# Optimization experiments

Measured on AMD Instinct MI355X. Metric: run time of the kernel, lower is better.

The kernel has to match this reference:

```python
import jax, jax.numpy as jnp
import numpy as np


def _ap_class_loss(s_plus, s_minus):
    """AP rank loss for one class.

    s_plus:  [P] positive scores sorted DESCENDING (grads flow through sort gather)
    s_minus: [N] negative scores sorted ASCENDING  (grads flow through sort gather)

    The original torch code computes the optimal interleaving rank of each
    negative with a recursive quickselect divide-and-conquer. Because the
    optimal rank is monotone in the negative's score (the property the
    divide-and-conquer exploits), each negative's rank can equivalently be
    computed independently: for the negative of ascending rank j (1-indexed),
    delta_k = 1/(P*(j+k)) - 2*(s_plus[k-1] - s_minus[j-1])/(P*N),  k=1..P,
    opt_j = argmax over r in [1, P+1] of sum_{k>=r} delta_k (first max on ties),
    which is exactly opt_j() evaluated on the full range.
    """
    P = s_plus.shape[0]
    N = s_minus.shape[0]
    Pf, Nf = float(P), float(N)
    j = jnp.arange(1, N + 1, dtype=jnp.float32)[:, None]   # [N,1] ascending rank
    k = jnp.arange(1, P + 1, dtype=jnp.float32)[None, :]   # [1,P]
    # delta[m, k-1] for negative m (ascending) vs positive k (descending)
    delta = (1.0 / (j + k)) / Pf - 2.0 * (s_plus[None, :] - s_minus[:, None]) / (Pf * Nf)
    dz = jnp.concatenate([delta, jnp.zeros((N, 1), delta.dtype)], axis=1)  # [N,P+1]
    # suffix[m, u] = sum_{i>=u} dz[m, i]  (matches flip-cumsum-flip in torch)
    suffix = jnp.cumsum(dz[:, ::-1], axis=1)[:, ::-1]
    opt = 1 + jnp.argmax(suffix, axis=1)                    # [N] int in [1, P+1]
    opt_f = jax.lax.stop_gradient(opt.astype(jnp.float32))
    # r_plus[i] = 1 + |{m : opt_m <= i+1}| via cumulative histogram of opt values
    hist = jnp.zeros(P + 2, jnp.float32).at[opt].add(1.0)
    cum = jnp.cumsum(hist)
    r_plus = 1.0 + cum[1:P + 1]                             # [P], thresholds 1..P
    i_arr = jnp.arange(P, dtype=jnp.float32)
    Delta_R_R_star = 1.0 - jnp.sum((i_arr + 1.0) / (i_arr + r_plus)) / Pf
    c_plus = Nf + 2.0 - 2.0 * r_plus                        # detached in torch
    c_minus = Pf + 2.0 - 2.0 * opt_f
    F_R = jnp.dot(s_plus, c_plus) + jnp.dot(s_minus, c_minus)
    # c_plus_star = N*ones, c_minus_star = -P*ones
    F_R_star = Nf * jnp.sum(s_plus) - Pf * jnp.sum(s_minus)
    return jax.lax.stop_gradient(Delta_R_R_star) + (F_R - F_R_star) / (Pf * Nf)


def _ap_loss(scores, pos_neg):
    total = jnp.zeros((), scores.dtype)
    for c, (pos, neg) in enumerate(pos_neg):
        if pos.size == 0 or neg.size == 0:
            continue  # torch returns 0 * s_plus.sum()
        col = scores[:, c]
        sp = col[pos]
        sm = col[neg]
        sp = sp[jnp.argsort(-sp)]   # descending; detached sort idx, grad via gather
        sm = sm[jnp.argsort(sm)]    # ascending (quickselect partial sort, same pairing)
        total = total + _ap_class_loss(sp, sm)
    return total / len(pos_neg)


def setup_inputs() -> dict:
    key = jax.random.key(0)
    k1, k2 = jax.random.split(key)
    C, n_classes = 16384, 16
    scores = jax.random.normal(k1, (C, n_classes), dtype=jnp.float32)
    class_labels = jax.random.randint(k2, (C,), 0, n_classes, dtype=jnp.int32)
    return {"scores": scores, "class_labels": class_labels}


def reference(scores, class_labels):
    labels = np.asarray(class_labels)
    n_classes = scores.shape[1]
    pos_neg = [(np.nonzero(labels == c)[0], np.nonzero(labels != c)[0])
               for c in range(n_classes)]
    return _ap_loss(scores, pos_neg)
```

## Files before the change

### kernel.cpp

```cpp
#include <hip/hip_runtime.h>
#include <stdint.h>

#define C_ITEMS 16384
#define NCLS 16
#define HSTRIDE 16386

static const size_t OFF_COL  = 0;
static const size_t OFF_SPOS = 1u << 20;
static const size_t OFF_SNEG = 2u << 20;
static const size_t OFF_PACK = 3u << 20;
static const size_t OFF_HIST = 4u << 20;
static const size_t OFF_CNT  = OFF_HIST + (size_t)NCLS * HSTRIDE * 4;
static const size_t OFF_ACCS = OFF_CNT + 64;
static const size_t OFF_ACCV = OFF_ACCS + 128;
static const size_t OFF_TOT  = OFF_ACCV + 128;
static const size_t OFF_PC   = OFF_TOT + 8;
static const size_t OFF_H1   = (OFF_PC + 64 + 255) & ~(size_t)255;
static const size_t OFF_PPK  = OFF_H1 + (((size_t)NCLS << 16) * 4);
static const size_t ZERO_BYTES = OFF_PPK - OFF_HIST;

__device__ __forceinline__ unsigned ordkey(float f) {
  unsigned b = __float_as_uint(f);
  return (b & 0x80000000u) ? ~b : (b | 0x80000000u);
}

__global__ void k_zero(unsigned* p, int n) {
  int stride = gridDim.x * blockDim.x;
  for (int t = blockIdx.x * blockDim.x + threadIdx.x; t < n; t += stride) p[t] = 0u;
}

__global__ void k_prep(const float* __restrict__ scores, const int* __restrict__ labels,
                       float* __restrict__ col, unsigned* __restrict__ h1) {
  int t = blockIdx.x * 256 + threadIdx.x;
  float v = scores[t];
  int i = t >> 4, c = t & 15;
  col[(c << 14) | i] = v;
  if (labels[i] != c)
    atomicAdd(&h1[(c << 16) + (ordkey(v) >> 16)], 1u);
}

__global__ void k_poscollect(const float* __restrict__ scores, const int* __restrict__ labels,
                             unsigned* __restrict__ pcnt, unsigned long long* __restrict__ ppk) {
  __shared__ unsigned lc[NCLS];
  __shared__ unsigned base[NCLS];
  int tid = threadIdx.x;
  if (tid < NCLS) lc[tid] = 0;
  __syncthreads();
  int i = blockIdx.x * 256 + tid;
  int c = labels[i] & 15;
  float v = scores[i * NCLS + c];
  unsigned loc = atomicAdd(&lc[c], 1u);
  __syncthreads();
  if (tid < NCLS) base[tid] = lc[tid] ? atomicAdd(&pcnt[tid], lc[tid]) : 0u;
  __syncthreads();
  ppk[(c << 14) + base[c] + loc] = ((unsigned long long)(~ordkey(v)) << 32) | (unsigned)i;
}

#define PCAP 4096
__global__ void k_posrank2(const float* __restrict__ scores,
                           const unsigned long long* __restrict__ ppk,
                           const unsigned* __restrict__ pcnt, float* __restrict__ spos) {
  int c = blockIdx.y;
  unsigned P = pcnt[c];
  int tid = threadIdx.x;
  __shared__ unsigned long long pk[PCAP];
  const unsigned long long* src = ppk + ((size_t)c << 14);
  if (P <= PCAP) {
    for (unsigned t = tid; t < P; t += 256) pk[t] = src[t];
    __syncthreads();
    for (unsigned q = blockIdx.x * 256 + tid; q < P; q += gridDim.x * 256) {
      unsigned long long k64 = pk[q];
      unsigned cq = 0;
      for (unsigned t = 0; t < P; ++t) cq += (pk[t] < k64) ? 1u : 0u;
      unsigned i = (unsigned)(k64 & 0xFFFFFFFFu);
      spos[(c << 14) + cq] = scores[i * NCLS + c];
    }
  } else {
    for (unsigned q = blockIdx.x * 256 + tid; q < P; q += gridDim.x * 256) {
      unsigned long long k64 = src[q];
      unsigned cq = 0;
      for (unsigned t = 0; t < P; ++t) cq += (src[t] < k64) ? 1u : 0u;
      unsigned i = (unsigned)(k64 & 0xFFFFFFFFu);
      spos[(c << 14) + cq] = scores[i * NCLS + c];
    }
  }
}

__global__ void k_scan1(unsigned* __restrict__ h1) {
  int c = blockIdx.x;
  unsigned* h = h1 + ((size_t)c << 16);
  int tid = threadIdx.x;
  unsigned base = (unsigned)tid << 6;
  unsigned s = 0;
  for (int q = 0; q < 64; ++q) s += h[base + q];
  __shared__ unsigned part[1024];
  part[tid] = s;
  __syncthreads();
  for (int off = 1; off < 1024; off <<= 1) {
    unsigned v = (tid >= off) ? part[tid - off] : 0u;
    __syncthreads();
    part[tid] += v;
    __syncthreads();
  }
  unsigned running = part[tid] - s;
  for (int q = 0; q < 64; ++q) {
    unsigned tmp = h[base + q];
    h[base + q] = running;
    running += tmp;
  }
}

__global__ void k_scatter(const float* __restrict__ col, const int* __restrict__ labels,
                          unsigned* __restrict__ h1, unsigned* __restrict__ pack) {
  int t = blockIdx.x * 256 + threadIdx.x;
  int c = t >> 14, i = t & 16383;
  if (labels[i] != c) {
    unsigned k = ordkey(col[t]);
    unsigned p = atomicAdd(&h1[(c << 16) + (k >> 16)], 1u);
    pack[(c << 14) + p] = (k << 16) | (unsigned)i;
  }
}

__global__ void k_rankfine(const float* __restrict__ col, const int* __restrict__ labels,
                           const unsigned* __restrict__ h1, const unsigned* __restrict__ pack,
                           float* __restrict__ sneg) {
  int t = blockIdx.x * 256 + threadIdx.x;
  int c = t >> 14, i = t & 16383;
  if (labels[i] != c) {
    float v = col[t];
    unsigned k = ordkey(v);
    unsigned b = k >> 16;
    const unsigned* hb = h1 + ((size_t)c << 16);
    unsigned start = b ? hb[b - 1] : 0u;
    unsigned end = hb[b];
    unsigned mine = (k << 16) | (unsigned)i;
    const unsigned* pk = pack + (c << 14);
    unsigned cnt = start;
    for (unsigned q = start; q < end; ++q) cnt += (pk[q] < mine) ? 1u : 0u;
    sneg[(c << 14) + cnt] = v;
  }
}

#define SCAP 2048
#define HCAP 2048
#define ABITS 6
#define ASTEP 64

__global__ void k_anchor(const unsigned* __restrict__ counts, const float* __restrict__ spos,
                         const float* __restrict__ sneg, unsigned* __restrict__ aopt) {
  int c = blockIdx.y;
  int P = (int)counts[c];
  int N = C_ITEMS - P;
  if (P == 0 || N == 0) return;
  int tid = threadIdx.x;
  __shared__ float sp[SCAP];
  int stageN = (P <= SCAP) ? P : 0;
  for (int t = tid; t < stageN; t += 256) sp[t] = spos[(c << 14) + t];
  __syncthreads();
  int T = (N + ASTEP - 1) / ASTEP + 1;
  float invP = 1.0f / (float)P;
  float coef = 2.0f / ((float)P * (float)N);
  for (int t = tid; t < T; t += 256) {
    int j0 = min(t * ASTEP, N - 1);
    float v = sneg[(c << 14) + j0];
    float a = coef * v;
    float fcnt = (float)(j0 + P + 1);
    float s = 0.0f, best = 0.0f;
    int besti = P;
    if (P <= SCAP) {
      for (int q = P - 1; q >= 0; --q) {
        float spv = sp[q];
        float r = __builtin_amdgcn_rcpf(fcnt);
        float delta = fmaf(invP, r, fmaf(-coef, spv, a));
        s += delta;
        if (s >= best) { best = s; besti = q; }
        fcnt -= 1.0f;
      }
    } else {
      const float* spg = spos + ((size_t)c << 14);
      for (int q = P - 1; q >= 0; --q) {
        float spv = spg[q];
        float r = __builtin_amdgcn_rcpf(fcnt);
        float delta = fmaf(invP, r, fmaf(-coef, spv, a));
        s += delta;
        if (s >= best) { best = s; besti = q; }
        fcnt -= 1.0f;
      }
    }
    aopt[(c << 9) + t] = (unsigned)(besti + 1);
  }
}

__global__ void k_optB(const unsigned* __restrict__ counts, const float* __restrict__ spos,
                       const float* __restrict__ sneg, const unsigned* __restrict__ aopt,
                       unsigned* __restrict__ hist, double* __restrict__ accS,
                       double* __restrict__ accV) {
  int c = blockIdx.y;
  int P = (int)counts[c];
  int N = C_ITEMS - P;
  if (P == 0 || N == 0) return;
  int tid = threadIdx.x;
  int j0 = blockIdx.x * 256 + tid;
  bool active = (j0 < N);
  __shared__ float sp[SCAP];
  __shared__ unsigned lh[HCAP];
  __shared__ double red[256];
  int stageN = (P <= SCAP) ? P : 0;
  for (int t = tid; t < stageN; t += 256) sp[t] = spos[(c << 14) + t];
  for (int t = tid; t < HCAP; t += 256) lh[t] = 0u;
  __syncthreads();
  int opt = P + 1;
  float v = 0.0f;
  if (active) {
    v = sneg[(c << 14) + j0];
    int g = j0 >> ABITS;
    int hiA = (int)aopt[(c << 9) + g];
    if ((j0 & (ASTEP - 1)) == 0) {
      opt = hiA;
    } else {
      int loA = (int)aopt[(c << 9) + g + 1];
      int hi = min(hiA + 2, P + 1);
      int lo = max(loA - 2, 1);
      float invP = 1.0f / (float)P;
      float coef = 2.0f / ((float)P * (float)N);
      float a = coef * v;
      float s = 0.0f, best = 0.0f;
      int bestr = hi;
      float fcnt = (float)(j0 + hi);
      if (P <= SCAP) {
        for (int k = hi - 1; k >= lo; --k) {
          float spv = sp[k - 1];
          float r = __builtin_amdgcn_rcpf(fcnt);
          float delta = fmaf(invP, r, fmaf(-coef, spv, a));
          s += delta;
          if (s >= best) { best = s; bestr = k; }
          fcnt -= 1.0f;
        }
      } else {
        const float* spg = spos + ((size_t)c << 14);
        for (int k = hi - 1; k >= lo; --k) {
          float spv = spg[k - 1];
          float r = __builtin_amdgcn_rcpf(fcnt);
          float delta = fmaf(invP, r, fmaf(-coef, spv, a));
          s += delta;
          if (s >= best) { best = s; bestr = k; }
          fcnt -= 1.0f;
        }
      }
      opt = bestr;
    }
  }
  if (P + 2 <= HCAP) {
    if (active) atomicAdd(&lh[opt], 1u);
    __syncthreads();
    for (int t = tid; t < P + 2; t += 256)
      if (lh[t]) atomicAdd(&hist[c * HSTRIDE + t], lh[t]);
  } else {
    if (active) atomicAdd(&hist[c * HSTRIDE + opt], 1u);
  }
  double cm = active ? (double)(P + 2 - 2 * opt) * (double)v : 0.0;
  double sv = active ? (double)v : 0.0;
  red[tid] = cm; __syncthreads();
  for (int sh = 128; sh > 0; sh >>= 1) { if (tid < sh) red[tid] += red[tid + sh]; __syncthreads(); }
  if (tid == 0) atomicAdd(&accS[c], red[0]);
  __syncthreads();
  red[tid] = sv; __syncthreads();
  for (int sh = 128; sh > 0; sh >>= 1) { if (tid < sh) red[tid] += red[tid + sh]; __syncthreads(); }
  if (tid == 0) atomicAdd(&accV[c], red[0]);
}

__global__ void k_finalize(const unsigned* __restrict__ counts, const unsigned* __restrict__ hist,
                           const float* __restrict__ spos, const double* __restrict__ accS,
                           const double* __restrict__ accV, double* __restrict__ total) {
  int c = blockIdx.x;
  int tid = threadIdx.x;
  int P = (int)counts[c];
  int N = C_ITEMS - P;
  if (P == 0 || N == 0) return;
  __shared__ unsigned sc[256];
  __shared__ double red[256];
  const unsigned* h = hist + c * HSTRIDE;
  int M = P + 1;
  int L = (M + 255) / 256;
  int o0 = 1 + tid * L;
  int o1 = min(o0 + L, P + 2);
  unsigned part = 0;
  for (int o = o0; o < o1; ++o) part += h[o];
  sc[tid] = part;
  __syncthreads();
  if (tid == 0) {
    unsigned runp = 0;
    for (int t = 0; t < 256; ++t) { unsigned tmp = sc[t]; sc[t] = runp; runp += tmp; }
  }
  __syncthreads();
  unsigned run = sc[tid];
  double a1 = 0.0, a2 = 0.0, a3 = 0.0;
  for (int o = o0; o < o1; ++o) {
    run += h[o];
    if (o <= P) {
      int k0 = o - 1;
      double rp = 1.0 + (double)run;
      double spv = (double)spos[(c << 14) + k0];
      a1 += (double)(k0 + 1) / ((double)k0 + rp);
      a2 += spv * ((double)N + 2.0 - 2.0 * rp);
      a3 += spv;
    }
  }
  red[tid] = a1; __syncthreads();
  for (int s = 128; s > 0; s >>= 1) { if (tid < s) red[tid] += red[tid + s]; __syncthreads(); }
  double r1 = red[0]; __syncthreads();
  red[tid] = a2; __syncthreads();
  for (int s = 128; s > 0; s >>= 1) { if (tid < s) red[tid] += red[tid + s]; __syncthreads(); }
  double r2 = red[0]; __syncthreads();
  red[tid] = a3; __syncthreads();
  for (int s = 128; s > 0; s >>= 1) { if (tid < s) red[tid] += red[tid + s]; __syncthreads(); }
  double r3 = red[0];
  if (tid == 0) {
    double Pd = (double)P, Nd = (double)N;
    double FR  = r2 + accS[c];
    double FRs = Nd * r3 - Pd * accV[c];
    double lc  = (1.0 - r1 / Pd) + (FR - FRs) / (Pd * Nd);
    atomicAdd(total, lc);
  }
}

__global__ void k_out(const double* __restrict__ total, float* __restrict__ out) {
  out[0] = (float)(total[0] / (double)NCLS);
}

extern "C" void kernel_launch(void* const* d_in, const int* in_sizes, int n_in,
                              void* d_out, int out_size, void* d_ws, size_t ws_size,
                              hipStream_t stream) {
  (void)in_sizes; (void)n_in; (void)out_size; (void)ws_size;
  const float* scores = (const float*)d_in[0];
  const int* labels = (const int*)d_in[1];
  float* out = (float*)d_out;
  char* ws = (char*)d_ws;
  float* col      = (float*)(ws + OFF_COL);
  float* spos     = (float*)(ws + OFF_SPOS);
  float* sneg     = (float*)(ws + OFF_SNEG);
  unsigned* pack  = (unsigned*)(ws + OFF_PACK);
  unsigned* hist  = (unsigned*)(ws + OFF_HIST);
  double* accS    = (double*)(ws + OFF_ACCS);
  double* accV    = (double*)(ws + OFF_ACCV);
  double* total   = (double*)(ws + OFF_TOT);
  unsigned* pcnt  = (unsigned*)(ws + OFF_PC);
  unsigned* h1    = (unsigned*)(ws + OFF_H1);
  unsigned long long* ppk = (unsigned long long*)(ws + OFF_PPK);
  unsigned* aopt  = (unsigned*)(ws + OFF_PPK);

  int zn = (int)(ZERO_BYTES / 4);
  k_zero<<<1024, 256, 0, stream>>>(hist, zn);
  k_prep<<<1024, 256, 0, stream>>>(scores, labels, col, h1);
  k_poscollect<<<64, 256, 0, stream>>>(scores, labels, pcnt, ppk);
  k_posrank2<<<dim3(16, NCLS), 256, 0, stream>>>(scores, ppk, pcnt, spos);
  k_scan1<<<NCLS, 1024, 0, stream>>>(h1);
  k_scatter<<<1024, 256, 0, stream>>>(col, labels, h1, pack);
  k_rankfine<<<1024, 256, 0, stream>>>(col, labels, h1, pack, sneg);
  k_anchor<<<dim3(1, NCLS), 256, 0, stream>>>(pcnt, spos, sneg, aopt);
  k_optB<<<dim3(64, NCLS), 256, 0, stream>>>(pcnt, spos, sneg, aopt, hist, accS, accV);
  k_finalize<<<NCLS, 256, 0, stream>>>(pcnt, hist, spos, accS, accV, total);
  k_out<<<1, 1, 0, stream>>>(total, out);
}
```

Baseline: 215.9 us.

## Fuse per-class sort, positive ranking and anchor search into one LDS-resident kernel

Merges the column transpose with positive collection, and collapses positive ranking, the negative radix histogram, scan, scatter, fine ranking and anchor search into one 1024-thread block per class that keeps its histogram and pack buffers in LDS. The final reduction and output write are folded together using a last-block counter. This is meant to remove launch overhead and global atomics/round-trips between stages. The cost is that only 16 blocks run the sort phase, which limits parallelism on a large GPU, and a large dynamic LDS allocation is required.

```diff
diff --git a/kernel.cpp b/kernel.cpp
--- a/kernel.cpp
+++ b/kernel.cpp
@@ -4,20 +4,22 @@
 #define C_ITEMS 16384
 #define NCLS 16
 #define HSTRIDE 16386
+#define NB 16384
+#define BSH 18
 
 static const size_t OFF_COL  = 0;
 static const size_t OFF_SPOS = 1u << 20;
 static const size_t OFF_SNEG = 2u << 20;
-static const size_t OFF_PACK = 3u << 20;
+static const size_t OFF_AOPT = 3u << 20;
 static const size_t OFF_HIST = 4u << 20;
 static const size_t OFF_CNT  = OFF_HIST + (size_t)NCLS * HSTRIDE * 4;
 static const size_t OFF_ACCS = OFF_CNT + 64;
 static const size_t OFF_ACCV = OFF_ACCS + 128;
 static const size_t OFF_TOT  = OFF_ACCV + 128;
 static const size_t OFF_PC   = OFF_TOT + 8;
-static const size_t OFF_H1   = (OFF_PC + 64 + 255) & ~(size_t)255;
-static const size_t OFF_PPK  = OFF_H1 + (((size_t)NCLS << 16) * 4);
-static const size_t ZERO_BYTES = OFF_PPK - OFF_HIST;
+static const size_t ZERO_END = OFF_PC + 64;
+static const size_t ZERO_BYTES = ZERO_END - OFF_HIST;
+static const size_t OFF_PPK  = 6u << 20;
 
 __device__ __forceinline__ unsigned ordkey(float f) {
   unsigned b = __float_as_uint(f);
@@ -29,168 +31,170 @@
   for (int t = blockIdx.x * blockDim.x + threadIdx.x; t < n; t += stride) p[t] = 0u;
 }
 
-__global__ void k_prep(const float* __restrict__ scores, const int* __restrict__ labels,
-                       float* __restrict__ col, unsigned* __restrict__ h1) {
-  int t = blockIdx.x * 256 + threadIdx.x;
-  float v = scores[t];
-  int i = t >> 4, c = t & 15;
-  col[(c << 14) | i] = v;
-  if (labels[i] != c)
-    atomicAdd(&h1[(c << 16) + (ordkey(v) >> 16)], 1u);
-}
-
-__global__ void k_poscollect(const float* __restrict__ scores, const int* __restrict__ labels,
-                             unsigned* __restrict__ pcnt, unsigned long long* __restrict__ ppk) {
+__global__ void k_prep2(const float* __restrict__ scores, const int* __restrict__ labels,
+                        float* __restrict__ col, unsigned* __restrict__ pcnt,
+                        unsigned long long* __restrict__ ppk) {
   __shared__ unsigned lc[NCLS];
   __shared__ unsigned base[NCLS];
   int tid = threadIdx.x;
   if (tid < NCLS) lc[tid] = 0;
   __syncthreads();
   int i = blockIdx.x * 256 + tid;
+  const float4* rp = (const float4*)(scores + (size_t)i * NCLS);
+  float4 r0 = rp[0], r1 = rp[1], r2 = rp[2], r3 = rp[3];
   int c = labels[i] & 15;
-  float v = scores[i * NCLS + c];
   unsigned loc = atomicAdd(&lc[c], 1u);
   __syncthreads();
   if (tid < NCLS) base[tid] = lc[tid] ? atomicAdd(&pcnt[tid], lc[tid]) : 0u;
   __syncthreads();
+  float v = scores[(size_t)i * NCLS + c];
   ppk[(c << 14) + base[c] + loc] = ((unsigned long long)(~ordkey(v)) << 32) | (unsigned)i;
-}
-
-#define PCAP 4096
-__global__ void k_posrank2(const float* __restrict__ scores,
-                           const unsigned long long* __restrict__ ppk,
-                           const unsigned* __restrict__ pcnt, float* __restrict__ spos) {
-  int c = blockIdx.y;
-  unsigned P = pcnt[c];
+  col[(0 << 14) + i] = r0.x;  col[(1 << 14) + i] = r0.y;
+  col[(2 << 14) + i] = r0.z;  col[(3 << 14) + i] = r0.w;
+  col[(4 << 14) + i] = r1.x;  col[(5 << 14) + i] = r1.y;
+  col[(6 << 14) + i] = r1.z;  col[(7 << 14) + i] = r1.w;
+  col[(8 << 14) + i] = r2.x;  col[(9 << 14) + i] = r2.y;
+  col[(10 << 14) + i] = r2.z; col[(11 << 14) + i] = r2.w;
+  col[(12 << 14) + i] = r3.x; col[(13 << 14) + i] = r3.y;
+  col[(14 << 14) + i] = r3.z; col[(15 << 14) + i] = r3.w;
+}
+
+#define SCAP 2048
+#define ASTEP 64
+#define ABITS 6
+
+extern __shared__ char smem_ms[];
+
+__global__ __launch_bounds__(1024) void k_megasort(
+    const float* __restrict__ col, const int* __restrict__ labels,
+    const unsigned* __restrict__ pcnt, const unsigned long long* __restrict__ ppk,
+    float* __restrict__ spos, float* __restrict__ sneg, unsigned* __restrict__ aopt) {
+  int c = blockIdx.x;
   int tid = threadIdx.x;
-  __shared__ unsigned long long pk[PCAP];
-  const unsigned long long* src = ppk + ((size_t)c << 14);
-  if (P <= PCAP) {
-    for (unsigned t = tid; t < P; t += 256) pk[t] = src[t];
-    __syncthreads();
-    for (unsigned q = blockIdx.x * 256 + tid; q < P; q += gridDim.x * 256) {
+  int P = (int)pcnt[c];
+  int N = C_ITEMS - P;
+  unsigned* hist = (unsigned*)smem_ms;
+  unsigned* pack = (unsigned*)(smem_ms + (size_t)NB * 4);
+  float*    sp   = (float*)(smem_ms + (size_t)NB * 4 + 65536);
+  unsigned long long* pk = (unsigned long long*)pack;
+  __shared__ unsigned part[1024];
+
+  bool small = (P > 0 && P <= SCAP);
+  if (small) {
+    const unsigned long long* src = ppk + ((size_t)c << 14);
+    for (int t = tid; t < P; t += 1024) pk[t] = src[t];
+    __syncthreads();
+    for (int q = tid; q < P; q += 1024) {
       unsigned long long k64 = pk[q];
       unsigned cq = 0;
-      for (unsigned t = 0; t < P; ++t) cq += (pk[t] < k64) ? 1u : 0u;
+      for (int t = 0; t < P; ++t) cq += (pk[t] < k64) ? 1u : 0u;
       unsigned i = (unsigned)(k64 & 0xFFFFFFFFu);
-      spos[(c << 14) + cq] = scores[i * NCLS + c];
-    }
-  } else {
-    for (unsigned q = blockIdx.x * 256 + tid; q < P; q += gridDim.x * 256) {
+      float v = col[(c << 14) + (int)i];
+      sp[cq] = v;
+      spos[(c << 14) + (int)cq] = v;
+    }
+  } else if (P > 0) {
+    const unsigned long long* src = ppk + ((size_t)c << 14);
+    for (int q = tid; q < P; q += 1024) {
       unsigned long long k64 = src[q];
       unsigned cq = 0;
-      for (unsigned t = 0; t < P; ++t) cq += (src[t] < k64) ? 1u : 0u;
+      for (int t = 0; t < P; ++t) cq += (src[t] < k64) ? 1u : 0u;
       unsigned i = (unsigned)(k64 & 0xFFFFFFFFu);
-      spos[(c << 14) + cq] = scores[i * NCLS + c];
-    }
-  }
-}
-
-__global__ void k_scan1(unsigned* __restrict__ h1) {
-  int c = blockIdx.x;
-  unsigned* h = h1 + ((size_t)c << 16);
-  int tid = threadIdx.x;
-  unsigned base = (unsigned)tid << 6;
-  unsigned s = 0;
-  for (int q = 0; q < 64; ++q) s += h[base + q];
-  __shared__ unsigned part[1024];
-  part[tid] = s;
-  __syncthreads();
-  for (int off = 1; off < 1024; off <<= 1) {
-    unsigned v = (tid >= off) ? part[tid - off] : 0u;
-    __syncthreads();
-    part[tid] += v;
-    __syncthreads();
-  }
-  unsigned running = part[tid] - s;
-  for (int q = 0; q < 64; ++q) {
-    unsigned tmp = h[base + q];
-    h[base + q] = running;
-    running += tmp;
-  }
-}
-
-__global__ void k_scatter(const float* __restrict__ col, const int* __restrict__ labels,
-                          unsigned* __restrict__ h1, unsigned* __restrict__ pack) {
-  int t = blockIdx.x * 256 + threadIdx.x;
-  int c = t >> 14, i = t & 16383;
-  if (labels[i] != c) {
-    unsigned k = ordkey(col[t]);
-    unsigned p = atomicAdd(&h1[(c << 16) + (k >> 16)], 1u);
-    pack[(c << 14) + p] = (k << 16) | (unsigned)i;
-  }
-}
-
-__global__ void k_rankfine(const float* __restrict__ col, const int* __restrict__ labels,
-                           const unsigned* __restrict__ h1, const unsigned* __restrict__ pack,
-                           float* __restrict__ sneg) {
-  int t = blockIdx.x * 256 + threadIdx.x;
-  int c = t >> 14, i = t & 16383;
-  if (labels[i] != c) {
-    float v = col[t];
-    unsigned k = ordkey(v);
-    unsigned b = k >> 16;
-    const unsigned* hb = h1 + ((size_t)c << 16);
-    unsigned start = b ? hb[b - 1] : 0u;
-    unsigned end = hb[b];
-    unsigned mine = (k << 16) | (unsigned)i;
-    const unsigned* pk = pack + (c << 14);
-    unsigned cnt = start;
-    for (unsigned q = start; q < end; ++q) cnt += (pk[q] < mine) ? 1u : 0u;
-    sneg[(c << 14) + cnt] = v;
-  }
-}
-
-#define SCAP 2048
+      spos[(c << 14) + (int)cq] = col[(c << 14) + (int)i];
+    }
+  }
+  __syncthreads();
+
+  for (int b = tid; b < NB; b += 1024) hist[b] = 0u;
+  __syncthreads();
+  if (N > 0)
+    for (int i = tid; i < C_ITEMS; i += 1024)
+      if (labels[i] != c) atomicAdd(&hist[ordkey(col[(c << 14) + i]) >> BSH], 1u);
+  __syncthreads();
+
+  {
+    int base = tid * (NB / 1024);
+    unsigned s = 0;
+    for (int q = 0; q < NB / 1024; ++q) s += hist[base + q];
+    part[tid] = s;
+    __syncthreads();
+    for (int off = 1; off < 1024; off <<= 1) {
+      unsigned v = (tid >= off) ? part[tid - off] : 0u;
+      __syncthreads();
+      part[tid] += v;
+      __syncthreads();
+    }
+    unsigned running = part[tid] - s;
+    for (int q = 0; q < NB / 1024; ++q) {
+      unsigned tmp = hist[base + q];
+      hist[base + q] = running;
+      running += tmp;
+    }
+  }
+  __syncthreads();
+
+  if (N > 0)
+    for (int i = tid; i < C_ITEMS; i += 1024)
+      if (labels[i] != c) {
+        unsigned k = ordkey(col[(c << 14) + i]);
+        unsigned p = atomicAdd(&hist[k >> BSH], 1u);
+        pack[p] = (k << 14) | (unsigned)i;
+      }
+  __syncthreads();
+
+  if (N > 0)
+    for (int i = tid; i < C_ITEMS; i += 1024)
+      if (labels[i] != c) {
+        float v = col[(c << 14) + i];
+        unsigned k = ordkey(v);
+        unsigned b = k >> BSH;
+        unsigned start = b ? hist[b - 1] : 0u;
+        unsigned end = hist[b];
+        unsigned mine = (k << 14) | (unsigned)i;
+        unsigned cnt = start;
+        for (unsigned q = start; q < end; ++q) cnt += (pack[q] < mine) ? 1u : 0u;
+        sneg[(c << 14) + (int)cnt] = v;
+      }
+  __threadfence_block();
+  __syncthreads();
+
+  if (P > 0 && N > 0) {
+    int T = (N + ASTEP - 1) / ASTEP + 1;
+    float invP = 1.0f / (float)P;
+    float coef = 2.0f / ((float)P * (float)N);
+    for (int t = tid; t < T; t += 1024) {
+      int j0 = min(t * ASTEP, N - 1);
+      float v = sneg[(c << 14) + j0];
+      float a = coef * v;
+      float fcnt = (float)(j0 + P + 1);
+      float s = 0.0f, best = 0.0f;
+      int besti = P;
+      if (P <= SCAP) {
+        for (int q = P - 1; q >= 0; --q) {
+          float spv = sp[q];
+          float r = __builtin_amdgcn_rcpf(fcnt);
+          float delta = fmaf(invP, r, fmaf(-coef, spv, a));
+          s += delta;
+          if (s >= best) { best = s; besti = q; }
+          fcnt -= 1.0f;
+        }
+      } else {
+        const float* spg = spos + ((size_t)c << 14);
+        for (int q = P - 1; q >= 0; --q) {
+          float spv = spg[q];
+          float r = __builtin_amdgcn_rcpf(fcnt);
+          float delta = fmaf(invP, r, fmaf(-coef, spv, a));
+          s += delta;
+          if (s >= best) { best = s; besti = q; }
+          fcnt -= 1.0f;
+        }
+      }
+      aopt[(c << 9) + t] = (unsigned)(besti + 1);
+    }
+  }
+}
+
 #define HCAP 2048
-#define ABITS 6
-#define ASTEP 64
-
-__global__ void k_anchor(const unsigned* __restrict__ counts, const float* __restrict__ spos,
-                         const float* __restrict__ sneg, unsigned* __restrict__ aopt) {
-  int c = blockIdx.y;
-  int P = (int)counts[c];
-  int N = C_ITEMS - P;
-  if (P == 0 || N == 0) return;
-  int tid = threadIdx.x;
-  __shared__ float sp[SCAP];
-  int stageN = (P <= SCAP) ? P : 0;
-  for (int t = tid; t < stageN; t += 256) sp[t] = spos[(c << 14) + t];
-  __syncthreads();
-  int T = (N + ASTEP - 1) / ASTEP + 1;
-  float invP = 1.0f / (float)P;
-  float coef = 2.0f / ((float)P * (float)N);
-  for (int t = tid; t < T; t += 256) {
-    int j0 = min(t * ASTEP, N - 1);
-    float v = sneg[(c << 14) + j0];
-    float a = coef * v;
-    float fcnt = (float)(j0 + P + 1);
-    float s = 0.0f, best = 0.0f;
-    int besti = P;
-    if (P <= SCAP) {
-      for (int q = P - 1; q >= 0; --q) {
-        float spv = sp[q];
-        float r = __builtin_amdgcn_rcpf(fcnt);
-        float delta = fmaf(invP, r, fmaf(-coef, spv, a));
-        s += delta;
-        if (s >= best) { best = s; besti = q; }
-        fcnt -= 1.0f;
-      }
-    } else {
-      const float* spg = spos + ((size_t)c << 14);
-      for (int q = P - 1; q >= 0; --q) {
-        float spv = spg[q];
-        float r = __builtin_amdgcn_rcpf(fcnt);
-        float delta = fmaf(invP, r, fmaf(-coef, spv, a));
-        s += delta;
-        if (s >= best) { best = s; besti = q; }
-        fcnt -= 1.0f;
-      }
-    }
-    aopt[(c << 9) + t] = (unsigned)(besti + 1);
-  }
-}
-
 __global__ void k_optB(const unsigned* __restrict__ counts, const float* __restrict__ spos,
                        const float* __restrict__ sneg, const unsigned* __restrict__ aopt,
                        unsigned* __restrict__ hist, double* __restrict__ accS,
@@ -269,63 +273,70 @@
   if (tid == 0) atomicAdd(&accV[c], red[0]);
 }
 
-__global__ void k_finalize(const unsigned* __restrict__ counts, const unsigned* __restrict__ hist,
-                           const float* __restrict__ spos, const double* __restrict__ accS,
-                           const double* __restrict__ accV, double* __restrict__ total) {
+__global__ void k_fin(const unsigned* __restrict__ counts, const unsigned* __restrict__ hist,
+                      const float* __restrict__ spos, const double* __restrict__ accS,
+                      const double* __restrict__ accV, double* __restrict__ total,
+                      unsigned* __restrict__ done, float* __restrict__ out) {
   int c = blockIdx.x;
   int tid = threadIdx.x;
   int P = (int)counts[c];
   int N = C_ITEMS - P;
-  if (P == 0 || N == 0) return;
   __shared__ unsigned sc[256];
   __shared__ double red[256];
-  const unsigned* h = hist + c * HSTRIDE;
-  int M = P + 1;
-  int L = (M + 255) / 256;
-  int o0 = 1 + tid * L;
-  int o1 = min(o0 + L, P + 2);
-  unsigned part = 0;
-  for (int o = o0; o < o1; ++o) part += h[o];
-  sc[tid] = part;
-  __syncthreads();
+  double lc = 0.0;
+  if (P > 0 && N > 0) {
+    const unsigned* h = hist + c * HSTRIDE;
+    int M = P + 1;
+    int L = (M + 255) / 256;
+    int o0 = 1 + tid * L;
+    int o1 = min(o0 + L, P + 2);
+    unsigned part = 0;
+    for (int o = o0; o < o1; ++o) part += h[o];
+    sc[tid] = part;
+    __syncthreads();
+    if (tid == 0) {
+      unsigned runp = 0;
+      for (int t = 0; t < 256; ++t) { unsigned tmp = sc[t]; sc[t] = runp; runp += tmp; }
+    }
+    __syncthreads();
+    unsigned run = sc[tid];
+    double a1 = 0.0, a2 = 0.0, a3 = 0.0;
+    for (int o = o0; o < o1; ++o) {
+      run += h[o];
+      if (o <= P) {
+        int k0 = o - 1;
+        double rp = 1.0 + (double)run;
+        double spv = (double)spos[(c << 14) + k0];
+        a1 += (double)(k0 + 1) / ((double)k0 + rp);
+        a2 += spv * ((double)N + 2.0 - 2.0 * rp);
+        a3 += spv;
+      }
+    }
+    red[tid] = a1; __syncthreads();
+    for (int s = 128; s > 0; s >>= 1) { if (tid < s) red[tid] += red[tid + s]; __syncthreads(); }
+    double r1 = red[0]; __syncthreads();
+    red[tid] = a2; __syncthreads();
+    for (int s = 128; s > 0; s >>= 1) { if (tid < s) red[tid] += red[tid + s]; __syncthreads(); }
+    double r2 = red[0]; __syncthreads();
+    red[tid] = a3; __syncthreads();
+    for (int s = 128; s > 0; s >>= 1) { if (tid < s) red[tid] += red[tid + s]; __syncthreads(); }
+    double r3 = red[0];
+    if (tid == 0) {
+      double Pd = (double)P, Nd = (double)N;
+      double FR  = r2 + accS[c];
+      double FRs = Nd * r3 - Pd * accV[c];
+      lc = (1.0 - r1 / Pd) + (FR - FRs) / (Pd * Nd);
+    }
+  }
   if (tid == 0) {
-    unsigned runp = 0;
-    for (int t = 0; t < 256; ++t) { unsigned tmp = sc[t]; sc[t] = runp; runp += tmp; }
-  }
-  __syncthreads();
-  unsigned run = sc[tid];
-  double a1 = 0.0, a2 = 0.0, a3 = 0.0;
-  for (int o = o0; o < o1; ++o) {
-    run += h[o];
-    if (o <= P) {
-      int k0 = o - 1;
-      double rp = 1.0 + (double)run;
-      double spv = (double)spos[(c << 14) + k0];
-      a1 += (double)(k0 + 1) / ((double)k0 + rp);
-      a2 += spv * ((double)N + 2.0 - 2.0 * rp);
-      a3 += spv;
-    }
-  }
-  red[tid] = a1; __syncthreads();
-  for (int s = 128; s > 0; s >>= 1) { if (tid < s) red[tid] += red[tid + s]; __syncthreads(); }
-  double r1 = red[0]; __syncthreads();
-  red[tid] = a2; __syncthreads();
-  for (int s = 128; s > 0; s >>= 1) { if (tid < s) red[tid] += red[tid + s]; __syncthreads(); }
-  double r2 = red[0]; __syncthreads();
-  red[tid] = a3; __syncthreads();
-  for (int s = 128; s > 0; s >>= 1) { if (tid < s) red[tid] += red[tid + s]; __syncthreads(); }
-  double r3 = red[0];
-  if (tid == 0) {
-    double Pd = (double)P, Nd = (double)N;
-    double FR  = r2 + accS[c];
-    double FRs = Nd * r3 - Pd * accV[c];
-    double lc  = (1.0 - r1 / Pd) + (FR - FRs) / (Pd * Nd);
-    atomicAdd(total, lc);
-  }
-}
-
-__global__ void k_out(const double* __restrict__ total, float* __restrict__ out) {
-  out[0] = (float)(total[0] / (double)NCLS);
+    if (P > 0 && N > 0) atomicAdd(total, lc);
+    __threadfence();
+    unsigned d = atomicAdd(done, 1u);
+    if (d == NCLS - 1) {
+      double t = atomicAdd(total, 0.0);
+      out[0] = (float)(t / (double)NCLS);
+    }
+  }
 }
 
 extern "C" void kernel_launch(void* const* d_in, const int* in_sizes, int n_in,
@@ -339,26 +350,27 @@
   float* col      = (float*)(ws + OFF_COL);
   float* spos     = (float*)(ws + OFF_SPOS);
   float* sneg     = (float*)(ws + OFF_SNEG);
-  unsigned* pack  = (unsigned*)(ws + OFF_PACK);
+  unsigned* aopt  = (unsigned*)(ws + OFF_AOPT);
   unsigned* hist  = (unsigned*)(ws + OFF_HIST);
+  unsigned* done  = (unsigned*)(ws + OFF_CNT);
   double* accS    = (double*)(ws + OFF_ACCS);
   double* accV    = (double*)(ws + OFF_ACCV);
   double* total   = (double*)(ws + OFF_TOT);
   unsigned* pcnt  = (unsigned*)(ws + OFF_PC);
-  unsigned* h1    = (unsigned*)(ws + OFF_H1);
   unsigned long long* ppk = (unsigned long long*)(ws + OFF_PPK);
-  unsigned* aopt  = (unsigned*)(ws + OFF_PPK);
+
+  size_t msLds = (size_t)NB * 4 + 65536 + 8192;
+  static bool attr_done = false;
+  if (!attr_done) {
+    (void)hipFuncSetAttribute((const void*)k_megasort,
+                              hipFuncAttributeMaxDynamicSharedMemorySize, (int)msLds);
+    attr_done = true;
+  }
 
   int zn = (int)(ZERO_BYTES / 4);
-  k_zero<<<1024, 256, 0, stream>>>(hist, zn);
-  k_prep<<<1024, 256, 0, stream>>>(scores, labels, col, h1);
-  k_poscollect<<<64, 256, 0, stream>>>(scores, labels, pcnt, ppk);
-  k_posrank2<<<dim3(16, NCLS), 256, 0, stream>>>(scores, ppk, pcnt, spos);
-  k_scan1<<<NCLS, 1024, 0, stream>>>(h1);
-  k_scatter<<<1024, 256, 0, stream>>>(col, labels, h1, pack);
-  k_rankfine<<<1024, 256, 0, stream>>>(col, labels, h1, pack, sneg);
-  k_anchor<<<dim3(1, NCLS), 256, 0, stream>>>(pcnt, spos, sneg, aopt);
+  k_zero<<<256, 256, 0, stream>>>(hist, zn);
+  k_prep2<<<64, 256, 0, stream>>>(scores, labels, col, pcnt, ppk);
+  k_megasort<<<NCLS, 1024, msLds, stream>>>(col, labels, pcnt, ppk, spos, sneg, aopt);
   k_optB<<<dim3(64, NCLS), 256, 0, stream>>>(pcnt, spos, sneg, aopt, hist, accS, accV);
-  k_finalize<<<NCLS, 256, 0, stream>>>(pcnt, hist, spos, accS, accV, total);
-  k_out<<<1, 1, 0, stream>>>(total, out);
-}
+  k_fin<<<NCLS, 256, 0, stream>>>(pcnt, hist, spos, accS, accV, total, done, out);
+}
```

Result: slower. 240.5 us (+11.4%).

## Fuse prep kernels, shrink coarse histogram, split anchor across blocks, fold output write

Applied to the files above, without the earlier changes.

Merges the column transpose, coarse histogram and positive collection into one kernel that reads each score row with vector loads. The coarse histogram drops from 16 to 14 bits per class, so it fits a 256-thread scan, and that scan runs in the same launch as the positive ranking. The anchor pass is spread over more 64-thread blocks instead of one block per class. The final output division is folded into the finalize kernel with a last-block counter. The goal is fewer launches and more parallelism in the serial stages, at the cost of larger fine buckets in the rank step and a smaller shared-memory cap for positives.

```diff
diff --git a/kernel.cpp b/kernel.cpp
--- a/kernel.cpp
+++ b/kernel.cpp
@@ -4,6 +4,8 @@
 #define C_ITEMS 16384
 #define NCLS 16
 #define HSTRIDE 16386
+#define NB 16384
+#define BSH 18
 
 static const size_t OFF_COL  = 0;
 static const size_t OFF_SPOS = 1u << 20;
@@ -16,97 +18,98 @@
 static const size_t OFF_TOT  = OFF_ACCV + 128;
 static const size_t OFF_PC   = OFF_TOT + 8;
 static const size_t OFF_H1   = (OFF_PC + 64 + 255) & ~(size_t)255;
-static const size_t OFF_PPK  = OFF_H1 + (((size_t)NCLS << 16) * 4);
-static const size_t ZERO_BYTES = OFF_PPK - OFF_HIST;
+static const size_t ZERO_END = OFF_H1 + ((size_t)NCLS * NB * 4);
+static const size_t ZERO_BYTES = ZERO_END - OFF_HIST;
+static const size_t OFF_PPK  = 6656u << 10;
 
 __device__ __forceinline__ unsigned ordkey(float f) {
   unsigned b = __float_as_uint(f);
   return (b & 0x80000000u) ? ~b : (b | 0x80000000u);
 }
 
-__global__ void k_zero(unsigned* p, int n) {
+__global__ void k_zero(unsigned* __restrict__ p, int n) {
   int stride = gridDim.x * blockDim.x;
   for (int t = blockIdx.x * blockDim.x + threadIdx.x; t < n; t += stride) p[t] = 0u;
 }
 
-__global__ void k_prep(const float* __restrict__ scores, const int* __restrict__ labels,
-                       float* __restrict__ col, unsigned* __restrict__ h1) {
-  int t = blockIdx.x * 256 + threadIdx.x;
-  float v = scores[t];
-  int i = t >> 4, c = t & 15;
-  col[(c << 14) | i] = v;
-  if (labels[i] != c)
-    atomicAdd(&h1[(c << 16) + (ordkey(v) >> 16)], 1u);
-}
-
-__global__ void k_poscollect(const float* __restrict__ scores, const int* __restrict__ labels,
-                             unsigned* __restrict__ pcnt, unsigned long long* __restrict__ ppk) {
+__global__ void k_prep2(const float* __restrict__ scores, const int* __restrict__ labels,
+                        float* __restrict__ col, unsigned* __restrict__ pcnt,
+                        unsigned long long* __restrict__ ppk, unsigned* __restrict__ h1) {
   __shared__ unsigned lc[NCLS];
   __shared__ unsigned base[NCLS];
   int tid = threadIdx.x;
   if (tid < NCLS) lc[tid] = 0;
   __syncthreads();
   int i = blockIdx.x * 256 + tid;
+  const float4* rp = (const float4*)(scores + (size_t)i * NCLS);
+  float4 r0 = rp[0], r1 = rp[1], r2 = rp[2], r3 = rp[3];
+  float vals[16] = {r0.x, r0.y, r0.z, r0.w, r1.x, r1.y, r1.z, r1.w,
+                    r2.x, r2.y, r2.z, r2.w, r3.x, r3.y, r3.z, r3.w};
   int c = labels[i] & 15;
-  float v = scores[i * NCLS + c];
   unsigned loc = atomicAdd(&lc[c], 1u);
   __syncthreads();
   if (tid < NCLS) base[tid] = lc[tid] ? atomicAdd(&pcnt[tid], lc[tid]) : 0u;
   __syncthreads();
+  float v = vals[c];
   ppk[(c << 14) + base[c] + loc] = ((unsigned long long)(~ordkey(v)) << 32) | (unsigned)i;
-}
-
-#define PCAP 4096
-__global__ void k_posrank2(const float* __restrict__ scores,
-                           const unsigned long long* __restrict__ ppk,
-                           const unsigned* __restrict__ pcnt, float* __restrict__ spos) {
-  int c = blockIdx.y;
-  unsigned P = pcnt[c];
-  int tid = threadIdx.x;
-  __shared__ unsigned long long pk[PCAP];
-  const unsigned long long* src = ppk + ((size_t)c << 14);
-  if (P <= PCAP) {
-    for (unsigned t = tid; t < P; t += 256) pk[t] = src[t];
+#pragma unroll
+  for (int cc = 0; cc < NCLS; ++cc) {
+    col[(cc << 14) + i] = vals[cc];
+    if (cc != c) atomicAdd(&h1[(cc << 14) + (ordkey(vals[cc]) >> BSH)], 1u);
+  }
+}
+
+#define PCAP 2048
+__global__ void k_mid(unsigned* __restrict__ h1, const float* __restrict__ col,
+                      const unsigned* __restrict__ pcnt,
+                      const unsigned long long* __restrict__ ppk,
+                      float* __restrict__ spos) {
+  int b = blockIdx.x;
+  int tid = threadIdx.x;
+  if (b < NCLS) {
+    unsigned* h = h1 + ((size_t)b << 14);
+    __shared__ unsigned part[256];
+    unsigned base = (unsigned)tid << 6;
+    unsigned s = 0;
+    for (int q = 0; q < 64; ++q) s += h[base + q];
+    part[tid] = s;
     __syncthreads();
-    for (unsigned q = blockIdx.x * 256 + tid; q < P; q += gridDim.x * 256) {
-      unsigned long long k64 = pk[q];
-      unsigned cq = 0;
-      for (unsigned t = 0; t < P; ++t) cq += (pk[t] < k64) ? 1u : 0u;
-      unsigned i = (unsigned)(k64 & 0xFFFFFFFFu);
-      spos[(c << 14) + cq] = scores[i * NCLS + c];
+    for (int off = 1; off < 256; off <<= 1) {
+      unsigned v = (tid >= off) ? part[tid - off] : 0u;
+      __syncthreads();
+      part[tid] += v;
+      __syncthreads();
+    }
+    unsigned running = part[tid] - s;
+    for (int q = 0; q < 64; ++q) {
+      unsigned tmp = h[base + q];
+      h[base + q] = running;
+      running += tmp;
     }
   } else {
-    for (unsigned q = blockIdx.x * 256 + tid; q < P; q += gridDim.x * 256) {
-      unsigned long long k64 = src[q];
-      unsigned cq = 0;
-      for (unsigned t = 0; t < P; ++t) cq += (src[t] < k64) ? 1u : 0u;
-      unsigned i = (unsigned)(k64 & 0xFFFFFFFFu);
-      spos[(c << 14) + cq] = scores[i * NCLS + c];
-    }
-  }
-}
-
-__global__ void k_scan1(unsigned* __restrict__ h1) {
-  int c = blockIdx.x;
-  unsigned* h = h1 + ((size_t)c << 16);
-  int tid = threadIdx.x;
-  unsigned base = (unsigned)tid << 6;
-  unsigned s = 0;
-  for (int q = 0; q < 64; ++q) s += h[base + q];
-  __shared__ unsigned part[1024];
-  part[tid] = s;
-  __syncthreads();
-  for (int off = 1; off < 1024; off <<= 1) {
-    unsigned v = (tid >= off) ? part[tid - off] : 0u;
-    __syncthreads();
-    part[tid] += v;
-    __syncthreads();
-  }
-  unsigned running = part[tid] - s;
-  for (int q = 0; q < 64; ++q) {
-    unsigned tmp = h[base + q];
-    h[base + q] = running;
-    running += tmp;
+    int c = (b - NCLS) >> 2, s4 = (b - NCLS) & 3;
+    unsigned P = pcnt[c];
+    __shared__ unsigned long long pk[PCAP];
+    const unsigned long long* src = ppk + ((size_t)c << 14);
+    if (P <= PCAP) {
+      for (unsigned t = tid; t < P; t += 256) pk[t] = src[t];
+      __syncthreads();
+      for (unsigned q = (unsigned)((tid << 2) + s4); q < P; q += 1024) {
+        unsigned long long k64 = pk[q];
+        unsigned cq = 0;
+        for (unsigned t = 0; t < P; ++t) cq += (pk[t] < k64) ? 1u : 0u;
+        unsigned i = (unsigned)(k64 & 0xFFFFFFFFu);
+        spos[(c << 14) + cq] = col[(c << 14) + (int)i];
+      }
+    } else {
+      for (unsigned q = (unsigned)((tid << 2) + s4); q < P; q += 1024) {
+        unsigned long long k64 = src[q];
+        unsigned cq = 0;
+        for (unsigned t = 0; t < P; ++t) cq += (src[t] < k64) ? 1u : 0u;
+        unsigned i = (unsigned)(k64 & 0xFFFFFFFFu);
+        spos[(c << 14) + cq] = col[(c << 14) + (int)i];
+      }
+    }
   }
 }
 
@@ -116,8 +119,8 @@
   int c = t >> 14, i = t & 16383;
   if (labels[i] != c) {
     unsigned k = ordkey(col[t]);
-    unsigned p = atomicAdd(&h1[(c << 16) + (k >> 16)], 1u);
-    pack[(c << 14) + p] = (k << 16) | (unsigned)i;
+    unsigned p = atomicAdd(&h1[(c << 14) + (k >> BSH)], 1u);
+    pack[(c << 14) + p] = (k << 14) | (unsigned)i;
   }
 }
 
@@ -129,22 +132,21 @@
   if (labels[i] != c) {
     float v = col[t];
     unsigned k = ordkey(v);
-    unsigned b = k >> 16;
-    const unsigned* hb = h1 + ((size_t)c << 16);
+    unsigned b = k >> BSH;
+    const unsigned* hb = h1 + ((size_t)c << 14);
     unsigned start = b ? hb[b - 1] : 0u;
     unsigned end = hb[b];
-    unsigned mine = (k << 16) | (unsigned)i;
+    unsigned mine = (k << 14) | (unsigned)i;
     const unsigned* pk = pack + (c << 14);
     unsigned cnt = start;
     for (unsigned q = start; q < end; ++q) cnt += (pk[q] < mine) ? 1u : 0u;
-    sneg[(c << 14) + cnt] = v;
+    sneg[(c << 14) + (int)cnt] = v;
   }
 }
 
 #define SCAP 2048
-#define HCAP 2048
+#define ASTEP 64
 #define ABITS 6
-#define ASTEP 64
 
 __global__ void k_anchor(const unsigned* __restrict__ counts, const float* __restrict__ spos,
                          const float* __restrict__ sneg, unsigned* __restrict__ aopt) {
@@ -155,42 +157,43 @@
   int tid = threadIdx.x;
   __shared__ float sp[SCAP];
   int stageN = (P <= SCAP) ? P : 0;
-  for (int t = tid; t < stageN; t += 256) sp[t] = spos[(c << 14) + t];
-  __syncthreads();
+  for (int t = tid; t < stageN; t += 64) sp[t] = spos[(c << 14) + t];
+  __syncthreads();
+  int ta = blockIdx.x * 64 + tid;
   int T = (N + ASTEP - 1) / ASTEP + 1;
+  if (ta >= T) return;
   float invP = 1.0f / (float)P;
   float coef = 2.0f / ((float)P * (float)N);
-  for (int t = tid; t < T; t += 256) {
-    int j0 = min(t * ASTEP, N - 1);
-    float v = sneg[(c << 14) + j0];
-    float a = coef * v;
-    float fcnt = (float)(j0 + P + 1);
-    float s = 0.0f, best = 0.0f;
-    int besti = P;
-    if (P <= SCAP) {
-      for (int q = P - 1; q >= 0; --q) {
-        float spv = sp[q];
-        float r = __builtin_amdgcn_rcpf(fcnt);
-        float delta = fmaf(invP, r, fmaf(-coef, spv, a));
-        s += delta;
-        if (s >= best) { best = s; besti = q; }
-        fcnt -= 1.0f;
-      }
-    } else {
-      const float* spg = spos + ((size_t)c << 14);
-      for (int q = P - 1; q >= 0; --q) {
-        float spv = spg[q];
-        float r = __builtin_amdgcn_rcpf(fcnt);
-        float delta = fmaf(invP, r, fmaf(-coef, spv, a));
-        s += delta;
-        if (s >= best) { best = s; besti = q; }
-        fcnt -= 1.0f;
-      }
-    }
-    aopt[(c << 9) + t] = (unsigned)(besti + 1);
-  }
-}
-
+  int j0 = min(ta * ASTEP, N - 1);
+  float v = sneg[(c << 14) + j0];
+  float a = coef * v;
+  float fcnt = (float)(j0 + P + 1);
+  float s = 0.0f, best = 0.0f;
+  int besti = P;
+  if (P <= SCAP) {
+    for (int q = P - 1; q >= 0; --q) {
+      float spv = sp[q];
+      float r = __builtin_amdgcn_rcpf(fcnt);
+      float delta = fmaf(invP, r, fmaf(-coef, spv, a));
+      s += delta;
+      if (s >= best) { best = s; besti = q; }
+      fcnt -= 1.0f;
+    }
+  } else {
+    const float* spg = spos + ((size_t)c << 14);
+    for (int q = P - 1; q >= 0; --q) {
+      float spv = spg[q];
+      float r = __builtin_amdgcn_rcpf(fcnt);
+      float delta = fmaf(invP, r, fmaf(-coef, spv, a));
+      s += delta;
+      if (s >= best) { best = s; besti = q; }
+      fcnt -= 1.0f;
+    }
+  }
+  aopt[(c << 9) + ta] = (unsigned)(besti + 1);
+}
+
+#define HCAP 2048
 __global__ void k_optB(const unsigned* __restrict__ counts, const float* __restrict__ spos,
                        const float* __restrict__ sneg, const unsigned* __restrict__ aopt,
                        unsigned* __restrict__ hist, double* __restrict__ accS,
@@ -206,8 +209,9 @@
   __shared__ unsigned lh[HCAP];
   __shared__ double red[256];
   int stageN = (P <= SCAP) ? P : 0;
+  int zn = (P + 2 <= HCAP) ? (P + 2) : 0;
   for (int t = tid; t < stageN; t += 256) sp[t] = spos[(c << 14) + t];
-  for (int t = tid; t < HCAP; t += 256) lh[t] = 0u;
+  for (int t = tid; t < zn; t += 256) lh[t] = 0u;
   __syncthreads();
   int opt = P + 1;
   float v = 0.0f;
@@ -269,63 +273,70 @@
   if (tid == 0) atomicAdd(&accV[c], red[0]);
 }
 
-__global__ void k_finalize(const unsigned* __restrict__ counts, const unsigned* __restrict__ hist,
-                           const float* __restrict__ spos, const double* __restrict__ accS,
-                           const double* __restrict__ accV, double* __restrict__ total) {
+__global__ void k_fin(const unsigned* __restrict__ counts, const unsigned* __restrict__ hist,
+                      const float* __restrict__ spos, const double* __restrict__ accS,
+                      const double* __restrict__ accV, double* __restrict__ total,
+                      unsigned* __restrict__ done, float* __restrict__ out) {
   int c = blockIdx.x;
   int tid = threadIdx.x;
   int P = (int)counts[c];
   int N = C_ITEMS - P;
-  if (P == 0 || N == 0) return;
   __shared__ unsigned sc[256];
   __shared__ double red[256];
-  const unsigned* h = hist + c * HSTRIDE;
-  int M = P + 1;
-  int L = (M + 255) / 256;
-  int o0 = 1 + tid * L;
-  int o1 = min(o0 + L, P + 2);
-  unsigned part = 0;
-  for (int o = o0; o < o1; ++o) part += h[o];
-  sc[tid] = part;
-  __syncthreads();
+  double lc = 0.0;
+  if (P > 0 && N > 0) {
+    const unsigned* h = hist + c * HSTRIDE;
+    int M = P + 1;
+    int L = (M + 255) / 256;
+    int o0 = 1 + tid * L;
+    int o1 = min(o0 + L, P + 2);
+    unsigned part = 0;
+    for (int o = o0; o < o1; ++o) part += h[o];
+    sc[tid] = part;
+    __syncthreads();
+    if (tid == 0) {
+      unsigned runp = 0;
+      for (int t = 0; t < 256; ++t) { unsigned tmp = sc[t]; sc[t] = runp; runp += tmp; }
+    }
+    __syncthreads();
+    unsigned run = sc[tid];
+    double a1 = 0.0, a2 = 0.0, a3 = 0.0;
+    for (int o = o0; o < o1; ++o) {
+      run += h[o];
+      if (o <= P) {
+        int k0 = o - 1;
+        double rp = 1.0 + (double)run;
+        double spv = (double)spos[(c << 14) + k0];
+        a1 += (double)(k0 + 1) / ((double)k0 + rp);
+        a2 += spv * ((double)N + 2.0 - 2.0 * rp);
+        a3 += spv;
+      }
+    }
+    red[tid] = a1; __syncthreads();
+    for (int s = 128; s > 0; s >>= 1) { if (tid < s) red[tid] += red[tid + s]; __syncthreads(); }
+    double r1 = red[0]; __syncthreads();
+    red[tid] = a2; __syncthreads();
+    for (int s = 128; s > 0; s >>= 1) { if (tid < s) red[tid] += red[tid + s]; __syncthreads(); }
+    double r2 = red[0]; __syncthreads();
+    red[tid] = a3; __syncthreads();
+    for (int s = 128; s > 0; s >>= 1) { if (tid < s) red[tid] += red[tid + s]; __syncthreads(); }
+    double r3 = red[0];
+    if (tid == 0) {
+      double Pd = (double)P, Nd = (double)N;
+      double FR  = r2 + accS[c];
+      double FRs = Nd * r3 - Pd * accV[c];
+      lc = (1.0 - r1 / Pd) + (FR - FRs) / (Pd * Nd);
+    }
+  }
   if (tid == 0) {
-    unsigned runp = 0;
-    for (int t = 0; t < 256; ++t) { unsigned tmp = sc[t]; sc[t] = runp; runp += tmp; }
-  }
-  __syncthreads();
-  unsigned run = sc[tid];
-  double a1 = 0.0, a2 = 0.0, a3 = 0.0;
-  for (int o = o0; o < o1; ++o) {
-    run += h[o];
-    if (o <= P) {
-      int k0 = o - 1;
-      double rp = 1.0 + (double)run;
-      double spv = (double)spos[(c << 14) + k0];
-      a1 += (double)(k0 + 1) / ((double)k0 + rp);
-      a2 += spv * ((double)N + 2.0 - 2.0 * rp);
-      a3 += spv;
-    }
-  }
-  red[tid] = a1; __syncthreads();
-  for (int s = 128; s > 0; s >>= 1) { if (tid < s) red[tid] += red[tid + s]; __syncthreads(); }
-  double r1 = red[0]; __syncthreads();
-  red[tid] = a2; __syncthreads();
-  for (int s = 128; s > 0; s >>= 1) { if (tid < s) red[tid] += red[tid + s]; __syncthreads(); }
-  double r2 = red[0]; __syncthreads();
-  red[tid] = a3; __syncthreads();
-  for (int s = 128; s > 0; s >>= 1) { if (tid < s) red[tid] += red[tid + s]; __syncthreads(); }
-  double r3 = red[0];
-  if (tid == 0) {
-    double Pd = (double)P, Nd = (double)N;
-    double FR  = r2 + accS[c];
-    double FRs = Nd * r3 - Pd * accV[c];
-    double lc  = (1.0 - r1 / Pd) + (FR - FRs) / (Pd * Nd);
-    atomicAdd(total, lc);
-  }
-}
-
-__global__ void k_out(const double* __restrict__ total, float* __restrict__ out) {
-  out[0] = (float)(total[0] / (double)NCLS);
+    if (P > 0 && N > 0) atomicAdd(total, lc);
+    __threadfence();
+    unsigned d = atomicAdd(done, 1u);
+    if (d == NCLS - 1) {
+      double t = atomicAdd(total, 0.0);
+      out[0] = (float)(t / (double)NCLS);
+    }
+  }
 }
 
 extern "C" void kernel_launch(void* const* d_in, const int* in_sizes, int n_in,
@@ -341,6 +352,7 @@
   float* sneg     = (float*)(ws + OFF_SNEG);
   unsigned* pack  = (unsigned*)(ws + OFF_PACK);
   unsigned* hist  = (unsigned*)(ws + OFF_HIST);
+  unsigned* done  = (unsigned*)(ws + OFF_CNT);
   double* accS    = (double*)(ws + OFF_ACCS);
   double* accV    = (double*)(ws + OFF_ACCV);
   double* total   = (double*)(ws + OFF_TOT);
@@ -350,15 +362,12 @@
   unsigned* aopt  = (unsigned*)(ws + OFF_PPK);
 
   int zn = (int)(ZERO_BYTES / 4);
-  k_zero<<<1024, 256, 0, stream>>>(hist, zn);
-  k_prep<<<1024, 256, 0, stream>>>(scores, labels, col, h1);
-  k_poscollect<<<64, 256, 0, stream>>>(scores, labels, pcnt, ppk);
-  k_posrank2<<<dim3(16, NCLS), 256, 0, stream>>>(scores, ppk, pcnt, spos);
-  k_scan1<<<NCLS, 1024, 0, stream>>>(h1);
+  k_zero<<<512, 256, 0, stream>>>(hist, zn);
+  k_prep2<<<64, 256, 0, stream>>>(scores, labels, col, pcnt, ppk, h1);
+  k_mid<<<80, 256, 0, stream>>>(h1, col, pcnt, ppk, spos);
   k_scatter<<<1024, 256, 0, stream>>>(col, labels, h1, pack);
   k_rankfine<<<1024, 256, 0, stream>>>(col, labels, h1, pack, sneg);
-  k_anchor<<<dim3(1, NCLS), 256, 0, stream>>>(pcnt, spos, sneg, aopt);
+  k_anchor<<<dim3(5, NCLS), 64, 0, stream>>>(pcnt, spos, sneg, aopt);
   k_optB<<<dim3(64, NCLS), 256, 0, stream>>>(pcnt, spos, sneg, aopt, hist, accS, accV);
-  k_finalize<<<NCLS, 256, 0, stream>>>(pcnt, hist, spos, accS, accV, total);
-  k_out<<<1, 1, 0, stream>>>(total, out);
-}
+  k_fin<<<NCLS, 256, 0, stream>>>(pcnt, hist, spos, accS, accV, total, done, out);
+}
```

New measurement: 237.0 us. 1.1x slower.
